# Optimization experiments

Measured on AMD Instinct MI355X. Metric: run time of the kernel, lower is better.

The kernel has to match this reference:

```python
import jax, jax.numpy as jnp
import numpy as np

N = 50000      # nodes
E = 800000     # edges (avg degree 16)
G = 128        # graphs in batch
IN = 128       # in_channels
H = 128        # hidden_dim
C = 10         # num_classes


def setup_inputs() -> dict:
    key = jax.random.key(0)
    ks = jax.random.split(key, 8)
    x = jax.random.normal(ks[0], (N, IN), dtype=jnp.float32)
    edge_index = jax.random.randint(ks[1], (2, E), 0, N)
    edge_attr = jax.random.uniform(ks[2], (E,), dtype=jnp.float32)
    batch = jnp.sort(jax.random.randint(ks[3], (N,), 0, G))
    def glorot(k, fan_in, fan_out):
        return jax.random.normal(k, (fan_in, fan_out), dtype=jnp.float32) / np.float32(np.sqrt(fan_in))
    return {
        "x": x,
        "edge_index": edge_index,
        "edge_attr": edge_attr,
        "batch": batch,
        "W1": glorot(ks[4], IN, H), "b1": jnp.zeros((H,), jnp.float32),
        "W2": glorot(ks[5], H, H), "b2": jnp.zeros((H,), jnp.float32),
        "W3": glorot(ks[6], H, C), "b3": jnp.zeros((C,), jnp.float32),
    }


def gcn_conv(x, src, dst, ew, W, b, n):
    # symmetric GCN normalization (self-loops already appended, weight 1)
    deg = jax.ops.segment_sum(ew, dst, num_segments=n)            # [N]
    dinv = jnp.where(deg > 0, jax.lax.rsqrt(deg), 0.0)
    norm = dinv[src] * ew * dinv[dst]                             # [E+N]
    h = x @ W                                                     # [N, out]
    agg = jax.ops.segment_sum(h[src] * norm[:, None], dst, num_segments=n)
    return agg + b


def reference(x, edge_index, edge_attr, batch, W1, b1, W2, b2, W3, b3):
    n = x.shape[0]
    loop = jnp.arange(n)
    src = jnp.concatenate([edge_index[0], loop])
    dst = jnp.concatenate([edge_index[1], loop])
    ew = jnp.concatenate([edge_attr, jnp.ones((n,), edge_attr.dtype)])
    h = jax.nn.relu(gcn_conv(x, src, dst, ew, W1, b1, n))   # dropout is identity in eval
    h = jax.nn.relu(gcn_conv(h, src, dst, ew, W2, b2, n))
    h = gcn_conv(h, src, dst, ew, W3, b3, n)                 # [N, C]
    # global mean pool over graphs
    sums = jax.ops.segment_sum(h, batch, num_segments=G)     # [G, C]
    cnt = jax.ops.segment_sum(jnp.ones((n,), h.dtype), batch, num_segments=G)
    pooled = sums / jnp.maximum(cnt, 1.0)[:, None]
    return jax.nn.log_softmax(pooled, axis=1)
```

## Files before the change

kernel.cpp:

```cpp
#include <hip/hip_runtime.h>

#define NN 50000
#define NE 800000
#define NG 128
#define DIM 128
#define CO 10
#define CAP 64
#define NB 2048

#define BKT_SHIFT 7
#define BKT_NODES 128
#define NBKT 391
#define NSEG 8
#define SEGCAP 448

typedef unsigned long long ull;
typedef unsigned short ushort;
typedef unsigned int uint;
typedef __attribute__((ext_vector_type(8))) short short8;
typedef __attribute__((ext_vector_type(4))) float floatx4;

static __device__ __forceinline__ ushort f2bf(float f) {
    uint u = __float_as_uint(f);
    uint r = (u + 0x7FFF + ((u >> 16) & 1)) >> 16;
    return (ushort)r;
}
#define EWS (1.0f / 65535.0f)
#define DGS (1.0f / 65536.0f)

__global__ void k_bucket(const int* __restrict__ src, const int* __restrict__ dst,
                         const float* __restrict__ ew, uint* __restrict__ bcnt,
                         ull* __restrict__ bkt) {
    int e = blockIdx.x * blockDim.x + threadIdx.x;
    if (e >= NE) return;
    int d = dst[e], s = src[e];
    float w = ew[e];
    int b = d >> BKT_SHIFT;
    int sb = b * NSEG + (blockIdx.x & 7);
    uint pos = atomicAdd(&bcnt[sb * 16], 1u);
    if (pos < SEGCAP) {
        ull rec = ((ull)__float_as_uint(w) << 32)
                | ((uint)(d & (BKT_NODES - 1)) << 16) | (uint)s;
        bkt[(size_t)sb * SEGCAP + pos] = rec;
    }
}

__global__ __launch_bounds__(256) void k_ellbuild(const uint* __restrict__ bcnt,
                                                  const ull* __restrict__ bkt,
                                                  ull* __restrict__ combo,
                                                  uint* __restrict__ ell) {
    __shared__ uint  lell[BKT_NODES * CAP];
    __shared__ uint  lcnt[BKT_NODES];
    __shared__ float ldeg[BKT_NODES];
    int b = blockIdx.x, tid = threadIdx.x;
    for (int i = tid; i < BKT_NODES; i += 256) { lcnt[i] = 0; ldeg[i] = 0.0f; }
    __syncthreads();
    for (int seg = 0; seg < NSEG; seg++) {
        int sb = b * NSEG + seg;
        uint n = min(bcnt[sb * 16], (uint)SEGCAP);
        const ull* base = &bkt[(size_t)sb * SEGCAP];
        for (uint r = tid; r < n; r += 256) {
            ull rec = base[r];
            uint lo = (uint)rec;
            float w = __uint_as_float((uint)(rec >> 32));
            uint doff = (lo >> 16) & 0xffu;
            uint s = lo & 0xffffu;
            uint slot = atomicAdd(&lcnt[doff], 1u);
            atomicAdd(&ldeg[doff], w);
            if (slot < CAP) {
                uint w16 = (uint)__float2uint_rn(w * 65535.0f);
                lell[doff * CAP + slot] = (w16 << 16) | s;
            }
        }
    }
    __syncthreads();
    int node0 = b * BKT_NODES;
    for (int i = tid; i < BKT_NODES; i += 256) {
        int node = node0 + i;
        if (node < NN) {
            uint dfix = (uint)__float2uint_rn(ldeg[i] * 65536.0f);
            combo[node] = ((ull)dfix << 32) | (ull)lcnt[i];
        }
    }
    int nvalid = min(NN - node0, BKT_NODES);
    int nvec = nvalid * CAP / 4;
    uint4* gdst = (uint4*)&ell[(size_t)node0 * CAP];
    const uint4* lsrc = (const uint4*)lell;
    for (int i = tid; i < nvec; i += 256) gdst[i] = lsrc[i];
}

__global__ void k_prepw(const float* __restrict__ W1, const float* __restrict__ W2,
                        ushort* __restrict__ wt1, ushort* __restrict__ wt2) {
    int b = blockIdx.x;
    const float* W = (b < 64) ? W1 : W2;
    ushort* Wt = (b < 64) ? wt1 : wt2;
    int i = (b & 63) * 256 + threadIdx.x;
    int k = i >> 7, n = i & 127;
    Wt[n * 128 + k] = f2bf(W[i]);
}

static __device__ __forceinline__ float combo_dinv(ull cb) {
    return rsqrtf(1.0f + (float)(uint)(cb >> 32) * DGS);
}

__global__ __launch_bounds__(256) void k_gemm_mfma(const void* __restrict__ Ain, int abf,
                                                   const ushort* __restrict__ Wt,
                                                   const ull* __restrict__ combo,
                                                   ushort* __restrict__ C, int M) {
    int wave = threadIdx.x >> 6;
    int lane = threadIdx.x & 63;
    int quad = lane >> 4;
    int mcol = lane & 15;
    int r0 = blockIdx.x * 64 + wave * 16;
    int arow = r0 + mcol;
    if (arow >= M) arow = M - 1;
    floatx4 acc[8];
#pragma unroll
    for (int t = 0; t < 8; t++) acc[t] = (floatx4){0.0f, 0.0f, 0.0f, 0.0f};

    const ushort* Ab = (const ushort*)Ain;
    const float*  Af = (const float*)Ain;
#pragma unroll
    for (int kk = 0; kk < 4; kk++) {
        int koff = kk * 32 + quad * 8;
        short8 a;
        if (abf) {
            a = *(const short8*)&Ab[(size_t)arow * 128 + koff];
        } else {
            const float* ap = &Af[(size_t)arow * 128 + koff];
            float4 x0 = *(const float4*)ap;
            float4 x1 = *(const float4*)(ap + 4);
            union { short8 v; ushort u[8]; } ua;
            ua.u[0] = f2bf(x0.x); ua.u[1] = f2bf(x0.y); ua.u[2] = f2bf(x0.z); ua.u[3] = f2bf(x0.w);
            ua.u[4] = f2bf(x1.x); ua.u[5] = f2bf(x1.y); ua.u[6] = f2bf(x1.z); ua.u[7] = f2bf(x1.w);
            a = ua.v;
        }
#pragma unroll
        for (int t = 0; t < 8; t++) {
            short8 b = *(const short8*)&Wt[(size_t)(t * 16 + mcol) * 128 + koff];
            acc[t] = __builtin_amdgcn_mfma_f32_16x16x32_bf16(a, b, acc[t], 0, 0, 0);
        }
    }
#pragma unroll
    for (int reg = 0; reg < 4; reg++) {
        int row = r0 + quad * 4 + reg;
        if (row < M) {
            float di = combo_dinv(combo[row]);
            ushort* cp = &C[(size_t)row * 128];
#pragma unroll
            for (int t = 0; t < 8; t++) cp[t * 16 + mcol] = f2bf(di * acc[t][reg]);
        }
    }
}

template<int FUSEZ>
__global__ __launch_bounds__(256) void k_gather_t(const ull* __restrict__ combo,
                                                  const uint* __restrict__ ell,
                                                  const ushort* __restrict__ h,
                                                  const float* __restrict__ b,
                                                  ushort* __restrict__ outp,
                                                  const float* __restrict__ W3,
                                                  float* __restrict__ z) {
    __shared__ float Ws[1280];
    if constexpr (FUSEZ) {
        for (int i = threadIdx.x; i < 1280; i += 256) {
            Ws[i] = W3[(i & 127) * 10 + (i >> 7)];
        }
        __syncthreads();
    }
    int node = blockIdx.x * 4 + (threadIdx.x >> 6);
    int lane = threadIdx.x & 63;
    if (node >= NN) return;
    ull cb = combo[node];
    int n = min((int)(uint)cb, 63);
    float dg = (float)(uint)(cb >> 32) * DGS;
    int ce; float we;
    if (lane < n) {
        uint rec = ell[(size_t)node * CAP + lane];
        ce = (int)(rec & 0xffffu);
        we = (float)(rec >> 16) * EWS;
    } else {
        ce = node;
        we = (lane == n) ? 1.0f : 0.0f;
    }
    int grp  = lane >> 4;
    int col8 = lane & 15;
    float acc[8];
#pragma unroll
    for (int f = 0; f < 8; f++) acc[f] = 0.0f;
    int nb = (n + 4) >> 2;
    for (int bi = 0; bi < nb; bi++) {
        int idx = (bi << 2) | grp;
        int s = __shfl(ce, idx);
        float w = __shfl(we, idx);
        uint4 p = *(const uint4*)&h[(size_t)s * 128 + col8 * 8];
        acc[0] += w * __uint_as_float(p.x << 16);
        acc[1] += w * __uint_as_float(p.x & 0xffff0000u);
        acc[2] += w * __uint_as_float(p.y << 16);
        acc[3] += w * __uint_as_float(p.y & 0xffff0000u);
        acc[4] += w * __uint_as_float(p.z << 16);
        acc[5] += w * __uint_as_float(p.z & 0xffff0000u);
        acc[6] += w * __uint_as_float(p.w << 16);
        acc[7] += w * __uint_as_float(p.w & 0xffff0000u);
    }
#pragma unroll
    for (int f = 0; f < 8; f++) {
        acc[f] += __shfl_xor(acc[f], 16);
        acc[f] += __shfl_xor(acc[f], 32);
    }
    float di = rsqrtf(1.0f + dg);
    if constexpr (!FUSEZ) {
        if (lane < 16) {
            union { ushort u[8]; uint4 v; } o;
#pragma unroll
            for (int f = 0; f < 8; f++) {
                float vv = fmaxf(di * acc[f] + b[col8 * 8 + f], 0.0f);
                o.u[f] = f2bf(vv);
            }
            *(uint4*)&outp[(size_t)node * 128 + col8 * 8] = o.v;
        }
    } else {
        float v[8];
#pragma unroll
        for (int f = 0; f < 8; f++)
            v[f] = fmaxf(di * acc[f] + b[col8 * 8 + f], 0.0f);
        int c0 = grp * 3;
        int fadd = (col8 >> 2) + 2 * grp;
#pragma unroll
        for (int j = 0; j < 3; j++) {
            int c = c0 + j;
            float p = 0.0f;
            if (c < 10) {
                const float* wrow = &Ws[c * 128 + col8 * 8];
#pragma unroll
                for (int t = 0; t < 8; t++) {
                    int f = (t + fadd) & 7;
                    p += v[f] * wrow[f];
                }
            }
            p += __shfl_xor(p, 1);
            p += __shfl_xor(p, 2);
            p += __shfl_xor(p, 4);
            p += __shfl_xor(p, 8);
            if (c < 10 && col8 == 0) z[(size_t)node * 10 + c] = di * p;
        }
    }
}

__global__ __launch_bounds__(256) void k_pool_node(const ull* __restrict__ combo,
                                                   const uint* __restrict__ ell,
                                                   const float* __restrict__ z,
                                                   const int* __restrict__ batch,
                                                   float* __restrict__ partial) {
    __shared__ float ls[NG * CO + NG];
    for (int i = threadIdx.x; i < NG * CO + NG; i += 256) ls[i] = 0.0f;
    __syncthreads();
    int lane = threadIdx.x & 63;
    int grp  = lane >> 4;
    int c    = lane & 15;
    int gwave = blockIdx.x * 4 + (threadIdx.x >> 6);
    for (int node = gwave; node < NN; node += NB * 4) {
        ull cb = combo[node];
        int n = min((int)(uint)cb, 63);
        int ce; float we;
        if (lane < n) {
            uint rec = ell[(size_t)node * CAP + lane];
            ce = (int)(rec & 0xffffu);
            we = (float)(rec >> 16) * EWS;
        } else {
            ce = node;
            we = (lane == n) ? 1.0f : 0.0f;
        }
        float acc = 0.0f;
        int nb = (n + 4) >> 2;
        for (int bi = 0; bi < nb; bi++) {
            int idx = (bi << 2) | grp;
            int s = __shfl(ce, idx);
            float w = __shfl(we, idx);
            float v = (c < 10) ? z[(size_t)s * 10 + c] : 0.0f;
            acc += w * v;
        }
        acc += __shfl_xor(acc, 16);
        acc += __shfl_xor(acc, 32);
        int g = batch[node];
        if (lane < 10) {
            float di = combo_dinv(cb);
            atomicAdd(&ls[g * 10 + lane], di * acc);
        } else if (lane == 10) {
            atomicAdd(&ls[NG * CO + g], 1.0f);
        }
    }
    __syncthreads();
    float* pb = &partial[(size_t)blockIdx.x * (NG * CO + NG)];
    for (int i = threadIdx.x; i < NG * CO + NG; i += 256) pb[i] = ls[i];
}

__global__ __launch_bounds__(256) void k_pool_final(const float* __restrict__ partial,
                                                    const float* __restrict__ b3,
                                                    float* __restrict__ out) {
    __shared__ float red[4][11];
    int g = blockIdx.x;
    int t = threadIdx.x;
    int lane = t & 63, wv = t >> 6;
    float v[10]; float c = 0.0f;
#pragma unroll
    for (int f = 0; f < 10; f++) v[f] = 0.0f;
    for (int b = t; b < NB; b += 256) {
        const float* pb = &partial[(size_t)b * (NG * CO + NG)];
#pragma unroll
        for (int f = 0; f < 10; f++) v[f] += pb[g * 10 + f];
        c += pb[NG * CO + g];
    }
#pragma unroll
    for (int off = 32; off; off >>= 1) {
#pragma unroll
        for (int f = 0; f < 10; f++) v[f] += __shfl_down(v[f], off);
        c += __shfl_down(c, off);
    }
    if (lane == 0) {
#pragma unroll
        for (int f = 0; f < 10; f++) red[wv][f] = v[f];
        red[wv][10] = c;
    }
    __syncthreads();
    if (t == 0) {
        float p[10], m = -1e30f;
        float cc = red[0][10] + red[1][10] + red[2][10] + red[3][10];
        cc = fmaxf(cc, 1.0f);
#pragma unroll
        for (int f = 0; f < 10; f++) {
            p[f] = (red[0][f] + red[1][f] + red[2][f] + red[3][f]) / cc + b3[f];
            m = fmaxf(m, p[f]);
        }
        float ssum = 0.0f;
#pragma unroll
        for (int f = 0; f < 10; f++) ssum += __expf(p[f] - m);
        float lse = m + __logf(ssum);
#pragma unroll
        for (int f = 0; f < 10; f++) out[g * 10 + f] = p[f] - lse;
    }
}

extern "C" void kernel_launch(void* const* d_in, const int* in_sizes, int n_in,
                              void* d_out, int out_size, void* d_ws, size_t ws_size,
                              hipStream_t stream) {
    const float* x     = (const float*)d_in[0];
    const int*   ei    = (const int*)d_in[1];
    const float* ea    = (const float*)d_in[2];
    const int*   batch = (const int*)d_in[3];
    const float* W1    = (const float*)d_in[4];
    const float* b1    = (const float*)d_in[5];
    const float* W2    = (const float*)d_in[6];
    const float* b2    = (const float*)d_in[7];
    const float* W3    = (const float*)d_in[8];
    const float* b3    = (const float*)d_in[9];
    float* out = (float*)d_out;
    float* ws  = (float*)d_ws;

    const int* esrc = ei;
    const int* edst = ei + NE;

    ushort* hb      = (ushort*)ws;
    ushort* gb      = (ushort*)(ws + 3200000);
    float*  z       = ws + 6400000;
    ull*    combo   = (ull*)(ws + 6900000);
    uint*   ell     = (uint*)(ws + 7000000);
    ushort* wt1     = (ushort*)(ws + 10200000);
    ushort* wt2     = (ushort*)(ws + 10210000);
    float*  partial = (float*)hb;
    ull*    bkt     = (ull*)gb;
    uint*   bcnt    = (uint*)z;

    hipMemsetAsync(bcnt, 0, (size_t)NBKT * NSEG * 16 * sizeof(uint), stream);
    k_bucket<<<(NE + 255) / 256, 256, 0, stream>>>(esrc, edst, ea, bcnt, bkt);
    k_ellbuild<<<NBKT, 256, 0, stream>>>(bcnt, bkt, combo, ell);
    k_prepw<<<128, 256, 0, stream>>>(W1, W2, wt1, wt2);

    k_gemm_mfma<<<(NN + 63) / 64, 256, 0, stream>>>(x, 0, wt1, combo, hb, NN);
    k_gather_t<0><<<(NN + 3) / 4, 256, 0, stream>>>(combo, ell, hb, b1, gb, nullptr, nullptr);

    k_gemm_mfma<<<(NN + 63) / 64, 256, 0, stream>>>(gb, 1, wt2, combo, hb, NN);
    k_gather_t<1><<<(NN + 3) / 4, 256, 0, stream>>>(combo, ell, hb, b2, nullptr, W3, z);

    k_pool_node<<<NB, 256, 0, stream>>>(combo, ell, z, batch, partial);
    k_pool_final<<<NG, 256, 0, stream>>>(partial, b3, out);
}
```

Measured before the change: 299.9 us.

## Store transformed features as int8 with per-row scales and prefetch gather rows

The GEMM epilogue now quantizes each output row to signed int8 with a per-row absmax scale, instead of writing bf16. The scale is found with a lane shuffle reduction and stored in a separate float array. The gather kernels read 8 bytes per lane instead of 16 and fold the row scale into the edge weight. The gather loop is also software-pipelined so the next neighbor row load is issued before the current one is accumulated. This halves the random-access traffic of the aggregation, at the cost of lower precision and an extra dependent scale load per edge.

```diff
diff --git a/kernel.cpp b/kernel.cpp
--- a/kernel.cpp
+++ b/kernel.cpp
@@ -17,6 +17,7 @@
 typedef unsigned long long ull;
 typedef unsigned short ushort;
 typedef unsigned int uint;
+typedef unsigned char uchar8_t;
 typedef __attribute__((ext_vector_type(8))) short short8;
 typedef __attribute__((ext_vector_type(4))) float floatx4;
 
@@ -106,7 +107,8 @@
 __global__ __launch_bounds__(256) void k_gemm_mfma(const void* __restrict__ Ain, int abf,
                                                    const ushort* __restrict__ Wt,
                                                    const ull* __restrict__ combo,
-                                                   ushort* __restrict__ C, int M) {
+                                                   uchar8_t* __restrict__ C8,
+                                                   float* __restrict__ hsc, int M) {
     int wave = threadIdx.x >> 6;
     int lane = threadIdx.x & 63;
     int quad = lane >> 4;
@@ -146,9 +148,24 @@
         int row = r0 + quad * 4 + reg;
         if (row < M) {
             float di = combo_dinv(combo[row]);
-            ushort* cp = &C[(size_t)row * 128];
-#pragma unroll
-            for (int t = 0; t < 8; t++) cp[t * 16 + mcol] = f2bf(di * acc[t][reg]);
+            float v[8]; float m = 0.0f;
+#pragma unroll
+            for (int t = 0; t < 8; t++) {
+                v[t] = di * acc[t][reg];
+                m = fmaxf(m, fabsf(v[t]));
+            }
+            m = fmaxf(m, __shfl_xor(m, 1));
+            m = fmaxf(m, __shfl_xor(m, 2));
+            m = fmaxf(m, __shfl_xor(m, 4));
+            m = fmaxf(m, __shfl_xor(m, 8));
+            float inv = (m > 0.0f) ? 127.0f / m : 0.0f;
+            if (mcol == 0) hsc[row] = m * (1.0f / 127.0f);
+            uchar8_t* cp = &C8[(size_t)row * 128];
+#pragma unroll
+            for (int t = 0; t < 8; t++) {
+                int q = __float2int_rn(v[t] * inv);
+                cp[t * 16 + mcol] = (uchar8_t)(signed char)q;
+            }
         }
     }
 }
@@ -156,7 +173,8 @@
 template<int FUSEZ>
 __global__ __launch_bounds__(256) void k_gather_t(const ull* __restrict__ combo,
                                                   const uint* __restrict__ ell,
-                                                  const ushort* __restrict__ h,
+                                                  const uchar8_t* __restrict__ h8,
+                                                  const float* __restrict__ hsc,
                                                   const float* __restrict__ b,
                                                   ushort* __restrict__ outp,
                                                   const float* __restrict__ W3,
@@ -189,20 +207,36 @@
 #pragma unroll
     for (int f = 0; f < 8; f++) acc[f] = 0.0f;
     int nb = (n + 4) >> 2;
-    for (int bi = 0; bi < nb; bi++) {
-        int idx = (bi << 2) | grp;
+    float wc;
+    uint2 pc;
+    {
+        int s = __shfl(ce, grp);
+        wc = __shfl(we, grp) * hsc[s];
+        pc = *(const uint2*)&h8[(size_t)s * 128 + col8 * 8];
+    }
+    for (int bi = 0; bi < nb - 1; bi++) {
+        int idx = ((bi + 1) << 2) | grp;
         int s = __shfl(ce, idx);
-        float w = __shfl(we, idx);
-        uint4 p = *(const uint4*)&h[(size_t)s * 128 + col8 * 8];
-        acc[0] += w * __uint_as_float(p.x << 16);
-        acc[1] += w * __uint_as_float(p.x & 0xffff0000u);
-        acc[2] += w * __uint_as_float(p.y << 16);
-        acc[3] += w * __uint_as_float(p.y & 0xffff0000u);
-        acc[4] += w * __uint_as_float(p.z << 16);
-        acc[5] += w * __uint_as_float(p.z & 0xffff0000u);
-        acc[6] += w * __uint_as_float(p.w << 16);
-        acc[7] += w * __uint_as_float(p.w & 0xffff0000u);
-    }
+        float wn = __shfl(we, idx) * hsc[s];
+        uint2 pn = *(const uint2*)&h8[(size_t)s * 128 + col8 * 8];
+        acc[0] += wc * (float)(int)(signed char)(pc.x);
+        acc[1] += wc * (float)(int)(signed char)(pc.x >> 8);
+        acc[2] += wc * (float)(int)(signed char)(pc.x >> 16);
+        acc[3] += wc * (float)(int)(signed char)(pc.x >> 24);
+        acc[4] += wc * (float)(int)(signed char)(pc.y);
+        acc[5] += wc * (float)(int)(signed char)(pc.y >> 8);
+        acc[6] += wc * (float)(int)(signed char)(pc.y >> 16);
+        acc[7] += wc * (float)(int)(signed char)(pc.y >> 24);
+        pc = pn; wc = wn;
+    }
+    acc[0] += wc * (float)(int)(signed char)(pc.x);
+    acc[1] += wc * (float)(int)(signed char)(pc.x >> 8);
+    acc[2] += wc * (float)(int)(signed char)(pc.x >> 16);
+    acc[3] += wc * (float)(int)(signed char)(pc.x >> 24);
+    acc[4] += wc * (float)(int)(signed char)(pc.y);
+    acc[5] += wc * (float)(int)(signed char)(pc.y >> 8);
+    acc[6] += wc * (float)(int)(signed char)(pc.y >> 16);
+    acc[7] += wc * (float)(int)(signed char)(pc.y >> 24);
 #pragma unroll
     for (int f = 0; f < 8; f++) {
         acc[f] += __shfl_xor(acc[f], 16);
@@ -360,14 +394,15 @@
     const int* esrc = ei;
     const int* edst = ei + NE;
 
-    ushort* hb      = (ushort*)ws;
+    uchar8_t* h8    = (uchar8_t*)ws;
+    float*  hsc     = ws + 1700000;
     ushort* gb      = (ushort*)(ws + 3200000);
     float*  z       = ws + 6400000;
     ull*    combo   = (ull*)(ws + 6900000);
     uint*   ell     = (uint*)(ws + 7000000);
     ushort* wt1     = (ushort*)(ws + 10200000);
     ushort* wt2     = (ushort*)(ws + 10210000);
-    float*  partial = (float*)hb;
+    float*  partial = (float*)ws;
     ull*    bkt     = (ull*)gb;
     uint*   bcnt    = (uint*)z;
 
@@ -376,11 +411,11 @@
     k_ellbuild<<<NBKT, 256, 0, stream>>>(bcnt, bkt, combo, ell);
     k_prepw<<<128, 256, 0, stream>>>(W1, W2, wt1, wt2);
 
-    k_gemm_mfma<<<(NN + 63) / 64, 256, 0, stream>>>(x, 0, wt1, combo, hb, NN);
-    k_gather_t<0><<<(NN + 3) / 4, 256, 0, stream>>>(combo, ell, hb, b1, gb, nullptr, nullptr);
-
-    k_gemm_mfma<<<(NN + 63) / 64, 256, 0, stream>>>(gb, 1, wt2, combo, hb, NN);
-    k_gather_t<1><<<(NN + 3) / 4, 256, 0, stream>>>(combo, ell, hb, b2, nullptr, W3, z);
+    k_gemm_mfma<<<(NN + 63) / 64, 256, 0, stream>>>(x, 0, wt1, combo, h8, hsc, NN);
+    k_gather_t<0><<<(NN + 3) / 4, 256, 0, stream>>>(combo, ell, h8, hsc, b1, gb, nullptr, nullptr);
+
+    k_gemm_mfma<<<(NN + 63) / 64, 256, 0, stream>>>(gb, 1, wt2, combo, h8, hsc, NN);
+    k_gather_t<1><<<(NN + 3) / 4, 256, 0, stream>>>(combo, ell, h8, hsc, b2, nullptr, W3, z);
 
     k_pool_node<<<NB, 256, 0, stream>>>(combo, ell, z, batch, partial);
     k_pool_final<<<NG, 256, 0, stream>>>(partial, b3, out);
```

Result: faster. 291.8 us, median of 2 (-2.7%).
